# Kernel tuning notes

Hardware: AMD Instinct MI355X
Metric: run time of the kernel (lower is better)

Reference implementation:

```python
import jax, jax.numpy as jnp
import numpy as np

N = 100000        # nodes per batch
B = 1             # batch_size
E = 3200000       # edges
IN_F = 128        # in_features
ATT = 128         # attention_dim
HEADS = 8
DK = ATT // HEADS
SLOPE = 0.2       # leaky_relu_slope


def setup_inputs() -> dict:
    key = jax.random.key(0)
    k1, k2, k3, k4 = jax.random.split(key, 4)
    x = jax.random.normal(k1, (B * N, IN_F), dtype=jnp.float32)
    edge = jax.random.randint(k2, (B, 2, E), 0, N)
    # xavier_normal with gain=1.414 on W:[IN_F, ATT]
    W = jax.random.normal(k3, (IN_F, ATT), dtype=jnp.float32) * (1.414 * np.sqrt(2.0 / (IN_F + ATT)))
    # a originally [1, 2*d_k, 1, 1]; flattened to [2*d_k] (same math)
    a = jax.random.normal(k4, (2 * DK,), dtype=jnp.float32) * (1.414 * np.sqrt(2.0 / (2 * DK + 1)))
    return {"x": x, "edge": edge, "W": W, "a": a}


def _segment_softmax(scores, seg):
    # scores: [E, H], seg: [E] -> softmax within each segment (node id)
    smax = jax.ops.segment_max(scores, seg, num_segments=N)
    ex = jnp.exp(scores - smax[seg])
    denom = jax.ops.segment_sum(ex, seg, num_segments=N)
    return ex / denom[seg]


def reference(x, edge, W, a):
    wx = x @ W                                           # [B*N, ATT]
    h = wx.reshape(B, N, HEADS, DK).transpose(0, 1, 3, 2)  # [B, N, DK, H]
    a1, a2 = a[:DK], a[DK:]
    # sum(a * concat(h_src, h_dst)) = a1.h_src + a2.h_dst (linearity)
    s_src = jnp.einsum('bnkh,k->bnh', h, a1)             # [B, N, H]
    s_dst = jnp.einsum('bnkh,k->bnh', h, a2)             # [B, N, H]
    src = edge[:, 0, :]                                  # [B, E]
    dst = edge[:, 1, :]                                  # [B, E]
    gather = jax.vmap(lambda s, i: s[i])
    scores = gather(s_src, src) + gather(s_dst, dst)     # [B, E, H]
    edge_e = jnp.where(scores > 0, scores, SLOPE * scores)  # leaky relu
    # attention_norm_idx = 0 -> normalize over edges sharing a source node
    attention = jax.vmap(_segment_softmax)(edge_e, src)  # [B, E, H]
    return attention, wx
```

## Files before the change

### kernel.cpp

```cpp
#include <hip/hip_runtime.h>

#define N_NODES 100000
#define E_EDGES 3200000
#define IN_F 128
#define ATT 128
#define HEADS 8
#define DK 16
#define SLOPE 0.2f
#define NH (N_NODES * HEADS)

#define CHUNK 1792
#define NCHUNK 56
#define NSPLIT 9
#define QCAP 1016
#define SCAN_THREADS 512
#define ROUND_EDGES (SCAN_THREADS * 32)

__global__ __launch_bounds__(256) void gemm_s_kernel(
    const float* __restrict__ x, const float* __restrict__ W,
    const float* __restrict__ a, float* __restrict__ wx,
    float* __restrict__ s_src, float* __restrict__ s_dst)
{
    __shared__ float xs[8][128];
    __shared__ float Ws[8][128];

    const int tid = threadIdx.x;
    const int ty  = tid >> 4;
    const int tx  = tid & 15;
    const int row0 = blockIdx.x * 128;

    float acc[8][8];
#pragma unroll
    for (int i = 0; i < 8; i++)
#pragma unroll
        for (int j = 0; j < 8; j++) acc[i][j] = 0.f;

    const int lrow  = tid >> 1;
    const int khalf = (tid & 1) * 4;
    const int wkk   = tid >> 5;
    const int wc    = (tid & 31) * 4;

    for (int k0 = 0; k0 < IN_F; k0 += 8) {
        float4 xv = make_float4(0.f, 0.f, 0.f, 0.f);
        const int grow = row0 + lrow;
        if (grow < N_NODES)
            xv = *(const float4*)(x + (size_t)grow * IN_F + k0 + khalf);
        const float4 wv = *(const float4*)(W + (size_t)(k0 + wkk) * ATT + wc);

        __syncthreads();
        xs[khalf + 0][lrow] = xv.x;
        xs[khalf + 1][lrow] = xv.y;
        xs[khalf + 2][lrow] = xv.z;
        xs[khalf + 3][lrow] = xv.w;
        *(float4*)(&Ws[wkk][wc]) = wv;
        __syncthreads();

#pragma unroll
        for (int kk = 0; kk < 8; kk++) {
            float av[8], bv[8];
            *(float4*)(av)     = *(const float4*)(&xs[kk][ty * 8]);
            *(float4*)(av + 4) = *(const float4*)(&xs[kk][ty * 8 + 4]);
            *(float4*)(bv)     = *(const float4*)(&Ws[kk][tx * 8]);
            *(float4*)(bv + 4) = *(const float4*)(&Ws[kk][tx * 8 + 4]);
#pragma unroll
            for (int r = 0; r < 8; r++)
#pragma unroll
                for (int c = 0; c < 8; c++)
                    acc[r][c] = fmaf(av[r], bv[c], acc[r][c]);
        }
    }

    const int koff = (tx & 1) * 8;
    const int head = tx >> 1;
    float a1[8], a2[8];
#pragma unroll
    for (int c = 0; c < 8; c++) {
        a1[c] = a[koff + c];
        a2[c] = a[DK + koff + c];
    }

#pragma unroll
    for (int r = 0; r < 8; r++) {
        const int grow = row0 + ty * 8 + r;
        const bool ok = (grow < N_NODES);
        if (ok) {
            *(float4*)(wx + (size_t)grow * ATT + tx * 8) =
                make_float4(acc[r][0], acc[r][1], acc[r][2], acc[r][3]);
            *(float4*)(wx + (size_t)grow * ATT + tx * 8 + 4) =
                make_float4(acc[r][4], acc[r][5], acc[r][6], acc[r][7]);
        }
        float p1 = 0.f, p2 = 0.f;
#pragma unroll
        for (int c = 0; c < 8; c++) {
            p1 = fmaf(acc[r][c], a1[c], p1);
            p2 = fmaf(acc[r][c], a2[c], p2);
        }
        p1 += __shfl_xor(p1, 1);
        p2 += __shfl_xor(p2, 1);
        if (((tx & 1) == 0) && ok) {
            s_src[(size_t)grow * HEADS + head] = p1;
            s_dst[(size_t)grow * HEADS + head] = p2;
        }
    }
}

__global__ __launch_bounds__(SCAN_THREADS) void denom_scan_kernel(
    const int* __restrict__ src, const int* __restrict__ dst,
    const float* __restrict__ s_src, const float* __restrict__ s_dst,
    float* __restrict__ denoms)
{
    __shared__ float acc[HEADS][CHUNK + 1];
    __shared__ int qs[QCAP];
    __shared__ int qe[QCAP];
    __shared__ int qc;

    const int t    = threadIdx.x;
    const int lane = t & 63;
    const int lo   = blockIdx.x * CHUNK;
    const int hi   = min(lo + CHUNK, N_NODES);
    const int split = blockIdx.y;

    for (int i = t; i < HEADS * (CHUNK + 1); i += SCAN_THREADS)
        ((float*)acc)[i] = 0.f;
    if (t == 0) qc = 0;
    __syncthreads();

    const int per_split = (E_EDGES + NSPLIT - 1) / NSPLIT;
    const int e0 = split * per_split;
    const int e1 = min(e0 + per_split, E_EDGES);
    const int nrounds = (e1 - e0 + ROUND_EDGES - 1) / ROUND_EDGES;

    for (int r = 0; r < nrounds; r++) {
        const int rb = e0 + r * ROUND_EDGES;
#pragma unroll
        for (int u = 0; u < 8; u++) {
            const int e4 = rb + (u * SCAN_THREADS + t) * 4;
            int4 s4 = make_int4(-1, -1, -1, -1);
            if (e4 < e1) s4 = *(const int4*)(src + e4);
            const int ss[4] = {s4.x, s4.y, s4.z, s4.w};
#pragma unroll
            for (int j = 0; j < 4; j++) {
                const int s = ss[j];
                const bool hit = (s >= lo) && (s < hi);
                const unsigned long long m = __ballot(hit);
                if (m) {
                    const int leader = __ffsll((long long)m) - 1;
                    int wb = 0;
                    if (lane == leader) wb = atomicAdd(&qc, __popcll(m));
                    wb = __shfl(wb, leader);
                    if (hit) {
                        const int idx = wb + __popcll(m & ((1ull << lane) - 1ull));
                        if (idx < QCAP) { qs[idx] = s; qe[idx] = e4 + j; }
                        else {
                            const int d = dst[e4 + j];
                            const float4* ps = (const float4*)(s_src + (size_t)s * HEADS);
                            const float4* pd = (const float4*)(s_dst + (size_t)d * HEADS);
                            const float4 a0 = ps[0], a1 = ps[1], b0 = pd[0], b1 = pd[1];
                            const float sc[8] = {a0.x + b0.x, a0.y + b0.y, a0.z + b0.z, a0.w + b0.w,
                                                 a1.x + b1.x, a1.y + b1.y, a1.z + b1.z, a1.w + b1.w};
#pragma unroll
                            for (int h = 0; h < 8; h++) {
                                float v = sc[h];
                                v = v > 0.f ? v : SLOPE * v;
                                atomicAdd(&acc[h][s - lo], __expf(v));
                            }
                        }
                    }
                }
            }
        }
        __syncthreads();
        const int nq = min(qc, QCAP);
        for (int base = 0; base < nq; base += SCAN_THREADS) {
            const int i = base + t;
            if (i < nq) {
                const int s = qs[i];
                const int d = dst[qe[i]];
                const float4* ps = (const float4*)(s_src + (size_t)s * HEADS);
                const float4* pd = (const float4*)(s_dst + (size_t)d * HEADS);
                const float4 a0 = ps[0], a1 = ps[1], b0 = pd[0], b1 = pd[1];
                const float sc[8] = {a0.x + b0.x, a0.y + b0.y, a0.z + b0.z, a0.w + b0.w,
                                     a1.x + b1.x, a1.y + b1.y, a1.z + b1.z, a1.w + b1.w};
#pragma unroll
                for (int h = 0; h < 8; h++) {
                    float v = sc[h];
                    v = v > 0.f ? v : SLOPE * v;
                    atomicAdd(&acc[h][s - lo], __expf(v));
                }
            }
        }
        __syncthreads();
        if (t == 0) qc = 0;
        __syncthreads();
    }

    const int cnt = (hi - lo) * HEADS;
    float* outp = denoms + (size_t)split * NH + (size_t)lo * HEADS;
    for (int i = t; i < cnt; i += SCAN_THREADS)
        outp[i] = acc[i & 7][i >> 3];
}

__global__ __launch_bounds__(256) void reduce_recip_kernel(float* __restrict__ denoms)
{
    const int i = blockIdx.x * 256 + threadIdx.x;
    if (i >= NH) return;
    float s = 0.f;
#pragma unroll
    for (int c = 0; c < NSPLIT; c++) s += denoms[(size_t)c * NH + i];
    denoms[i] = __frcp_rn(s);
}

__global__ __launch_bounds__(256) void norm_kernel(
    const int* __restrict__ src, const int* __restrict__ dst,
    const float* __restrict__ s_src, const float* __restrict__ s_dst,
    const float* __restrict__ rdenom, float* __restrict__ att)
{
    const int e = blockIdx.x * 256 + threadIdx.x;
    if (e >= E_EDGES) return;
    const int s = src[e];
    const int d = dst[e];
    const float4* ps = (const float4*)(s_src + (size_t)s * HEADS);
    const float4* pd = (const float4*)(s_dst + (size_t)d * HEADS);
    const float4 s0 = ps[0], s1 = ps[1], d0 = pd[0], d1 = pd[1];
    const float4* pr = (const float4*)(rdenom + (size_t)s * HEADS);
    const float4 r0 = pr[0], r1 = pr[1];
    float sc[8] = {s0.x + d0.x, s0.y + d0.y, s0.z + d0.z, s0.w + d0.w,
                   s1.x + d1.x, s1.y + d1.y, s1.z + d1.z, s1.w + d1.w};
    float rd[8] = {r0.x, r0.y, r0.z, r0.w, r1.x, r1.y, r1.z, r1.w};
    float o[8];
#pragma unroll
    for (int h = 0; h < 8; h++) {
        float v = sc[h];
        v = v > 0.f ? v : SLOPE * v;
        o[h] = __expf(v) * rd[h];
    }
    float4* po = (float4*)(att + (size_t)e * HEADS);
    po[0] = make_float4(o[0], o[1], o[2], o[3]);
    po[1] = make_float4(o[4], o[5], o[6], o[7]);
}

extern "C" void kernel_launch(void* const* d_in, const int* in_sizes, int n_in,
                              void* d_out, int out_size, void* d_ws, size_t ws_size,
                              hipStream_t stream)
{
    const float* x    = (const float*)d_in[0];
    const int*   edge = (const int*)d_in[1];
    const float* W    = (const float*)d_in[2];
    const float* a    = (const float*)d_in[3];

    float* out = (float*)d_out;
    float* att = out;
    float* wx  = out + (size_t)E_EDGES * HEADS;

    float* ws     = (float*)d_ws;
    float* s_src  = ws;
    float* s_dst  = s_src + (size_t)NH;
    float* denoms = s_dst + (size_t)NH;

    const int* src = edge;
    const int* dst = edge + E_EDGES;

    const int gemm_blocks = (N_NODES + 127) / 128;
    gemm_s_kernel<<<gemm_blocks, 256, 0, stream>>>(x, W, a, wx, s_src, s_dst);

    dim3 sgrid(NCHUNK, NSPLIT);
    denom_scan_kernel<<<sgrid, SCAN_THREADS, 0, stream>>>(src, dst, s_src, s_dst, denoms);

    const int nblocks = (NH + 255) / 256;
    reduce_recip_kernel<<<nblocks, 256, 0, stream>>>(denoms);

    const int eblocks = (E_EDGES + 255) / 256;
    norm_kernel<<<eblocks, 256, 0, stream>>>(src, dst, s_src, s_dst, denoms, att);
}
```

Baseline: 654.4 us.

## Bin edges by source chunk with histogram/scan/scatter before denominator accumulation

Replaces the per-chunk full edge scan, where each of the 56x9 blocks rereads all source indices and filters by ballot, with a counting-sort style binning. A histogram, prefix scan and scatter write packed (local src, dst) words into the attention output buffer as scratch. The denominator kernel then reads only its own bin's edges and accumulates exp scores in shared memory. This removes the redundant rereads of the edge array but adds three extra launches, a single-block scan, and scattered global writes.

```diff
diff --git a/kernel.cpp b/kernel.cpp
--- a/kernel.cpp
+++ b/kernel.cpp
@@ -9,12 +9,11 @@
 #define SLOPE 0.2f
 #define NH (N_NODES * HEADS)
 
-#define CHUNK 1792
-#define NCHUNK 56
-#define NSPLIT 9
-#define QCAP 1016
-#define SCAN_THREADS 512
-#define ROUND_EDGES (SCAN_THREADS * 32)
+#define CHUNK 896
+#define NBINS 112
+#define NS 8
+#define HB 512
+#define EPB 6272
 
 __global__ __launch_bounds__(256) void gemm_s_kernel(
     const float* __restrict__ x, const float* __restrict__ W,
@@ -104,100 +103,150 @@
     }
 }
 
-__global__ __launch_bounds__(SCAN_THREADS) void denom_scan_kernel(
+__global__ __launch_bounds__(256) void hist_kernel(
+    const int* __restrict__ src, int* __restrict__ counts)
+{
+    __shared__ int h[NBINS];
+    const int t = threadIdx.x;
+    const int b = blockIdx.x;
+    for (int i = t; i < NBINS; i += 256) h[i] = 0;
+    __syncthreads();
+
+    const int rb = b * EPB;
+    const int re = min(rb + EPB, E_EDGES);
+    for (int i = rb + t * 4; i < re; i += 256 * 4) {
+        const int4 s4 = *(const int4*)(src + i);
+        atomicAdd(&h[s4.x / CHUNK], 1);
+        atomicAdd(&h[s4.y / CHUNK], 1);
+        atomicAdd(&h[s4.z / CHUNK], 1);
+        atomicAdd(&h[s4.w / CHUNK], 1);
+    }
+    __syncthreads();
+    for (int i = t; i < NBINS; i += 256) counts[i * HB + b] = h[i];
+}
+
+__global__ __launch_bounds__(1024) void scan_kernel(
+    const int* __restrict__ counts, int* __restrict__ offs)
+{
+    __shared__ int part[1024];
+    const int t = threadIdx.x;
+    const int per = (NBINS * HB) / 1024;
+    const int base = t * per;
+
+    int sum = 0;
+    for (int i = 0; i < per; i++) sum += counts[base + i];
+    part[t] = sum;
+    __syncthreads();
+
+    for (int off = 1; off < 1024; off <<= 1) {
+        int v = 0;
+        if (t >= off) v = part[t - off];
+        __syncthreads();
+        if (t >= off) part[t] += v;
+        __syncthreads();
+    }
+
+    int run = (t == 0) ? 0 : part[t - 1];
+    for (int i = 0; i < per; i++) {
+        offs[base + i] = run;
+        run += counts[base + i];
+    }
+}
+
+__global__ __launch_bounds__(256) void scatter_kernel(
     const int* __restrict__ src, const int* __restrict__ dst,
+    const int* __restrict__ offs, unsigned int* __restrict__ binned)
+{
+    __shared__ int cur[NBINS];
+    const int t = threadIdx.x;
+    const int b = blockIdx.x;
+    for (int i = t; i < NBINS; i += 256) cur[i] = offs[i * HB + b];
+    __syncthreads();
+
+    const int rb = b * EPB;
+    const int re = min(rb + EPB, E_EDGES);
+    for (int i = rb + t * 4; i < re; i += 256 * 4) {
+        const int4 s4 = *(const int4*)(src + i);
+        const int4 d4 = *(const int4*)(dst + i);
+        const int ss[4] = {s4.x, s4.y, s4.z, s4.w};
+        const int dd[4] = {d4.x, d4.y, d4.z, d4.w};
+#pragma unroll
+        for (int j = 0; j < 4; j++) {
+            const int c = ss[j] / CHUNK;
+            const int pos = atomicAdd(&cur[c], 1);
+            binned[pos] = ((unsigned int)(ss[j] - c * CHUNK) << 17) |
+                          (unsigned int)dd[j];
+        }
+    }
+}
+
+__global__ __launch_bounds__(256, 4) void denom_binned_kernel(
+    const unsigned int* __restrict__ binned, const int* __restrict__ offs,
     const float* __restrict__ s_src, const float* __restrict__ s_dst,
     float* __restrict__ denoms)
 {
     __shared__ float acc[HEADS][CHUNK + 1];
-    __shared__ int qs[QCAP];
-    __shared__ int qe[QCAP];
-    __shared__ int qc;
-
-    const int t    = threadIdx.x;
-    const int lane = t & 63;
-    const int lo   = blockIdx.x * CHUNK;
-    const int hi   = min(lo + CHUNK, N_NODES);
-    const int split = blockIdx.y;
-
-    for (int i = t; i < HEADS * (CHUNK + 1); i += SCAN_THREADS)
+
+    const int t  = threadIdx.x;
+    const int c  = blockIdx.x;
+    const int j  = blockIdx.y;
+    const int lo = c * CHUNK;
+    const int hi = min(lo + CHUNK, N_NODES);
+
+    for (int i = t; i < HEADS * (CHUNK + 1); i += 256)
         ((float*)acc)[i] = 0.f;
-    if (t == 0) qc = 0;
-    __syncthreads();
-
-    const int per_split = (E_EDGES + NSPLIT - 1) / NSPLIT;
-    const int e0 = split * per_split;
-    const int e1 = min(e0 + per_split, E_EDGES);
-    const int nrounds = (e1 - e0 + ROUND_EDGES - 1) / ROUND_EDGES;
-
-    for (int r = 0; r < nrounds; r++) {
-        const int rb = e0 + r * ROUND_EDGES;
-#pragma unroll
-        for (int u = 0; u < 8; u++) {
-            const int e4 = rb + (u * SCAN_THREADS + t) * 4;
-            int4 s4 = make_int4(-1, -1, -1, -1);
-            if (e4 < e1) s4 = *(const int4*)(src + e4);
-            const int ss[4] = {s4.x, s4.y, s4.z, s4.w};
-#pragma unroll
-            for (int j = 0; j < 4; j++) {
-                const int s = ss[j];
-                const bool hit = (s >= lo) && (s < hi);
-                const unsigned long long m = __ballot(hit);
-                if (m) {
-                    const int leader = __ffsll((long long)m) - 1;
-                    int wb = 0;
-                    if (lane == leader) wb = atomicAdd(&qc, __popcll(m));
-                    wb = __shfl(wb, leader);
-                    if (hit) {
-                        const int idx = wb + __popcll(m & ((1ull << lane) - 1ull));
-                        if (idx < QCAP) { qs[idx] = s; qe[idx] = e4 + j; }
-                        else {
-                            const int d = dst[e4 + j];
-                            const float4* ps = (const float4*)(s_src + (size_t)s * HEADS);
-                            const float4* pd = (const float4*)(s_dst + (size_t)d * HEADS);
-                            const float4 a0 = ps[0], a1 = ps[1], b0 = pd[0], b1 = pd[1];
-                            const float sc[8] = {a0.x + b0.x, a0.y + b0.y, a0.z + b0.z, a0.w + b0.w,
-                                                 a1.x + b1.x, a1.y + b1.y, a1.z + b1.z, a1.w + b1.w};
-#pragma unroll
-                            for (int h = 0; h < 8; h++) {
-                                float v = sc[h];
-                                v = v > 0.f ? v : SLOPE * v;
-                                atomicAdd(&acc[h][s - lo], __expf(v));
-                            }
-                        }
-                    }
-                }
-            }
-        }
-        __syncthreads();
-        const int nq = min(qc, QCAP);
-        for (int base = 0; base < nq; base += SCAN_THREADS) {
-            const int i = base + t;
-            if (i < nq) {
-                const int s = qs[i];
-                const int d = dst[qe[i]];
-                const float4* ps = (const float4*)(s_src + (size_t)s * HEADS);
-                const float4* pd = (const float4*)(s_dst + (size_t)d * HEADS);
-                const float4 a0 = ps[0], a1 = ps[1], b0 = pd[0], b1 = pd[1];
-                const float sc[8] = {a0.x + b0.x, a0.y + b0.y, a0.z + b0.z, a0.w + b0.w,
-                                     a1.x + b1.x, a1.y + b1.y, a1.z + b1.z, a1.w + b1.w};
-#pragma unroll
-                for (int h = 0; h < 8; h++) {
-                    float v = sc[h];
-                    v = v > 0.f ? v : SLOPE * v;
-                    atomicAdd(&acc[h][s - lo], __expf(v));
-                }
-            }
-        }
-        __syncthreads();
-        if (t == 0) qc = 0;
-        __syncthreads();
-    }
+    __syncthreads();
+
+    const int start = offs[c * HB];
+    const int end   = (c + 1 < NBINS) ? offs[(c + 1) * HB] : E_EDGES;
+    const int len   = end - start;
+    const int e0 = start + (int)((long long)len * j / NS);
+    const int e1 = start + (int)((long long)len * (j + 1) / NS);
+
+    int i = e0 + t;
+    for (; i + 256 < e1; i += 512) {
+        const unsigned int w0 = binned[i];
+        const unsigned int w1 = binned[i + 256];
+        const int di0 = w0 & 0x1FFFF, sl0 = w0 >> 17;
+        const int di1 = w1 & 0x1FFFF, sl1 = w1 >> 17;
+        const float4* ps0 = (const float4*)(s_src + (size_t)(lo + sl0) * HEADS);
+        const float4* pd0 = (const float4*)(s_dst + (size_t)di0 * HEADS);
+        const float4* ps1 = (const float4*)(s_src + (size_t)(lo + sl1) * HEADS);
+        const float4* pd1 = (const float4*)(s_dst + (size_t)di1 * HEADS);
+        const float4 xa0 = ps0[0], xa1 = ps0[1], xb0 = pd0[0], xb1 = pd0[1];
+        const float4 ya0 = ps1[0], ya1 = ps1[1], yb0 = pd1[0], yb1 = pd1[1];
+        const float s0[8] = {xa0.x + xb0.x, xa0.y + xb0.y, xa0.z + xb0.z, xa0.w + xb0.w,
+                             xa1.x + xb1.x, xa1.y + xb1.y, xa1.z + xb1.z, xa1.w + xb1.w};
+        const float s1[8] = {ya0.x + yb0.x, ya0.y + yb0.y, ya0.z + yb0.z, ya0.w + yb0.w,
+                             ya1.x + yb1.x, ya1.y + yb1.y, ya1.z + yb1.z, ya1.w + yb1.w};
+#pragma unroll
+        for (int h = 0; h < 8; h++) {
+            float v0 = s0[h]; v0 = v0 > 0.f ? v0 : SLOPE * v0;
+            float v1 = s1[h]; v1 = v1 > 0.f ? v1 : SLOPE * v1;
+            atomicAdd(&acc[h][sl0], __expf(v0));
+            atomicAdd(&acc[h][sl1], __expf(v1));
+        }
+    }
+    if (i < e1) {
+        const unsigned int w0 = binned[i];
+        const int di0 = w0 & 0x1FFFF, sl0 = w0 >> 17;
+        const float4* ps0 = (const float4*)(s_src + (size_t)(lo + sl0) * HEADS);
+        const float4* pd0 = (const float4*)(s_dst + (size_t)di0 * HEADS);
+        const float4 xa0 = ps0[0], xa1 = ps0[1], xb0 = pd0[0], xb1 = pd0[1];
+        const float s0[8] = {xa0.x + xb0.x, xa0.y + xb0.y, xa0.z + xb0.z, xa0.w + xb0.w,
+                             xa1.x + xb1.x, xa1.y + xb1.y, xa1.z + xb1.z, xa1.w + xb1.w};
+#pragma unroll
+        for (int h = 0; h < 8; h++) {
+            float v0 = s0[h]; v0 = v0 > 0.f ? v0 : SLOPE * v0;
+            atomicAdd(&acc[h][sl0], __expf(v0));
+        }
+    }
+    __syncthreads();
 
     const int cnt = (hi - lo) * HEADS;
-    float* outp = denoms + (size_t)split * NH + (size_t)lo * HEADS;
-    for (int i = t; i < cnt; i += SCAN_THREADS)
-        outp[i] = acc[i & 7][i >> 3];
+    float* outp = denoms + (size_t)j * NH + (size_t)lo * HEADS;
+    for (int i2 = t; i2 < cnt; i2 += 256)
+        outp[i2] = acc[i2 & 7][i2 >> 3];
 }
 
 __global__ __launch_bounds__(256) void reduce_recip_kernel(float* __restrict__ denoms)
@@ -206,7 +255,7 @@
     if (i >= NH) return;
     float s = 0.f;
 #pragma unroll
-    for (int c = 0; c < NSPLIT; c++) s += denoms[(size_t)c * NH + i];
+    for (int c = 0; c < NS; c++) s += denoms[(size_t)c * NH + i];
     denoms[i] = __frcp_rn(s);
 }
 
@@ -256,6 +305,10 @@
     float* s_src  = ws;
     float* s_dst  = s_src + (size_t)NH;
     float* denoms = s_dst + (size_t)NH;
+    int*   counts = (int*)(denoms + (size_t)NS * NH);
+    int*   offs   = counts + (size_t)NBINS * HB;
+
+    unsigned int* binned = (unsigned int*)att;
 
     const int* src = edge;
     const int* dst = edge + E_EDGES;
@@ -263,8 +316,12 @@
     const int gemm_blocks = (N_NODES + 127) / 128;
     gemm_s_kernel<<<gemm_blocks, 256, 0, stream>>>(x, W, a, wx, s_src, s_dst);
 
-    dim3 sgrid(NCHUNK, NSPLIT);
-    denom_scan_kernel<<<sgrid, SCAN_THREADS, 0, stream>>>(src, dst, s_src, s_dst, denoms);
+    hist_kernel<<<HB, 256, 0, stream>>>(src, counts);
+    scan_kernel<<<1, 1024, 0, stream>>>(counts, offs);
+    scatter_kernel<<<HB, 256, 0, stream>>>(src, dst, offs, binned);
+
+    dim3 bgrid(NBINS, NS);
+    denom_binned_kernel<<<bgrid, 256, 0, stream>>>(binned, offs, s_src, s_dst, denoms);
 
     const int nblocks = (NH + 255) / 256;
     reduce_recip_kernel<<<nblocks, 256, 0, stream>>>(denoms);
```

Result: faster. 551.0 us (-15.8%).

## Replace chunked scan with fused exp-store and global atomic denominators

Applied to the files above, without the earlier changes.

Replaces the per-chunk edge scan (which rereads the source array once per node chunk) with a single pass per edge. That pass computes exp scores, stores them to the output, and accumulates softmax denominators via global float atomics. A later pass multiplies the stored values by reciprocal denominators. This removes repeated edge scanning and the split reduction, at the cost of an extra read/write of the attention output and heavy contended global atomics.

```diff
diff --git a/kernel.cpp b/kernel.cpp
--- a/kernel.cpp
+++ b/kernel.cpp
@@ -9,13 +9,6 @@
 #define SLOPE 0.2f
 #define NH (N_NODES * HEADS)
 
-#define CHUNK 1792
-#define NCHUNK 56
-#define NSPLIT 9
-#define QCAP 1016
-#define SCAN_THREADS 512
-#define ROUND_EDGES (SCAN_THREADS * 32)
-
 __global__ __launch_bounds__(256) void gemm_s_kernel(
     const float* __restrict__ x, const float* __restrict__ W,
     const float* __restrict__ a, float* __restrict__ wx,
@@ -104,139 +97,89 @@
     }
 }
 
-__global__ __launch_bounds__(SCAN_THREADS) void denom_scan_kernel(
+__global__ __launch_bounds__(256) void zero_kernel(float4* __restrict__ p)
+{
+    const int i = blockIdx.x * 256 + threadIdx.x;
+    if (i < NH / 4) p[i] = make_float4(0.f, 0.f, 0.f, 0.f);
+}
+
+__global__ __launch_bounds__(256) void edge_fused_kernel(
     const int* __restrict__ src, const int* __restrict__ dst,
     const float* __restrict__ s_src, const float* __restrict__ s_dst,
-    float* __restrict__ denoms)
-{
-    __shared__ float acc[HEADS][CHUNK + 1];
-    __shared__ int qs[QCAP];
-    __shared__ int qe[QCAP];
-    __shared__ int qc;
-
-    const int t    = threadIdx.x;
-    const int lane = t & 63;
-    const int lo   = blockIdx.x * CHUNK;
-    const int hi   = min(lo + CHUNK, N_NODES);
-    const int split = blockIdx.y;
-
-    for (int i = t; i < HEADS * (CHUNK + 1); i += SCAN_THREADS)
-        ((float*)acc)[i] = 0.f;
-    if (t == 0) qc = 0;
-    __syncthreads();
-
-    const int per_split = (E_EDGES + NSPLIT - 1) / NSPLIT;
-    const int e0 = split * per_split;
-    const int e1 = min(e0 + per_split, E_EDGES);
-    const int nrounds = (e1 - e0 + ROUND_EDGES - 1) / ROUND_EDGES;
-
-    for (int r = 0; r < nrounds; r++) {
-        const int rb = e0 + r * ROUND_EDGES;
-#pragma unroll
-        for (int u = 0; u < 8; u++) {
-            const int e4 = rb + (u * SCAN_THREADS + t) * 4;
-            int4 s4 = make_int4(-1, -1, -1, -1);
-            if (e4 < e1) s4 = *(const int4*)(src + e4);
-            const int ss[4] = {s4.x, s4.y, s4.z, s4.w};
-#pragma unroll
-            for (int j = 0; j < 4; j++) {
-                const int s = ss[j];
-                const bool hit = (s >= lo) && (s < hi);
-                const unsigned long long m = __ballot(hit);
-                if (m) {
-                    const int leader = __ffsll((long long)m) - 1;
-                    int wb = 0;
-                    if (lane == leader) wb = atomicAdd(&qc, __popcll(m));
-                    wb = __shfl(wb, leader);
-                    if (hit) {
-                        const int idx = wb + __popcll(m & ((1ull << lane) - 1ull));
-                        if (idx < QCAP) { qs[idx] = s; qe[idx] = e4 + j; }
-                        else {
-                            const int d = dst[e4 + j];
-                            const float4* ps = (const float4*)(s_src + (size_t)s * HEADS);
-                            const float4* pd = (const float4*)(s_dst + (size_t)d * HEADS);
-                            const float4 a0 = ps[0], a1 = ps[1], b0 = pd[0], b1 = pd[1];
-                            const float sc[8] = {a0.x + b0.x, a0.y + b0.y, a0.z + b0.z, a0.w + b0.w,
-                                                 a1.x + b1.x, a1.y + b1.y, a1.z + b1.z, a1.w + b1.w};
-#pragma unroll
-                            for (int h = 0; h < 8; h++) {
-                                float v = sc[h];
-                                v = v > 0.f ? v : SLOPE * v;
-                                atomicAdd(&acc[h][s - lo], __expf(v));
-                            }
-                        }
-                    }
-                }
-            }
-        }
-        __syncthreads();
-        const int nq = min(qc, QCAP);
-        for (int base = 0; base < nq; base += SCAN_THREADS) {
-            const int i = base + t;
-            if (i < nq) {
-                const int s = qs[i];
-                const int d = dst[qe[i]];
-                const float4* ps = (const float4*)(s_src + (size_t)s * HEADS);
-                const float4* pd = (const float4*)(s_dst + (size_t)d * HEADS);
-                const float4 a0 = ps[0], a1 = ps[1], b0 = pd[0], b1 = pd[1];
-                const float sc[8] = {a0.x + b0.x, a0.y + b0.y, a0.z + b0.z, a0.w + b0.w,
-                                     a1.x + b1.x, a1.y + b1.y, a1.z + b1.z, a1.w + b1.w};
-#pragma unroll
-                for (int h = 0; h < 8; h++) {
-                    float v = sc[h];
-                    v = v > 0.f ? v : SLOPE * v;
-                    atomicAdd(&acc[h][s - lo], __expf(v));
-                }
-            }
-        }
-        __syncthreads();
-        if (t == 0) qc = 0;
-        __syncthreads();
-    }
-
-    const int cnt = (hi - lo) * HEADS;
-    float* outp = denoms + (size_t)split * NH + (size_t)lo * HEADS;
-    for (int i = t; i < cnt; i += SCAN_THREADS)
-        outp[i] = acc[i & 7][i >> 3];
-}
-
-__global__ __launch_bounds__(256) void reduce_recip_kernel(float* __restrict__ denoms)
+    float* __restrict__ denoms, float* __restrict__ att)
+{
+    const int e0 = (blockIdx.x * 256 + threadIdx.x) * 2;
+    if (e0 >= E_EDGES) return;
+    const int2 sp = *(const int2*)(src + e0);
+    const int2 dp = *(const int2*)(dst + e0);
+
+    const float4* ps0 = (const float4*)(s_src + (size_t)sp.x * HEADS);
+    const float4* ps1 = (const float4*)(s_src + (size_t)sp.y * HEADS);
+    const float4* pd0 = (const float4*)(s_dst + (size_t)dp.x * HEADS);
+    const float4* pd1 = (const float4*)(s_dst + (size_t)dp.y * HEADS);
+    const float4 xa0 = ps0[0], xa1 = ps0[1];
+    const float4 ya0 = ps1[0], ya1 = ps1[1];
+    const float4 xb0 = pd0[0], xb1 = pd0[1];
+    const float4 yb0 = pd1[0], yb1 = pd1[1];
+
+    const float s0[8] = {xa0.x + xb0.x, xa0.y + xb0.y, xa0.z + xb0.z, xa0.w + xb0.w,
+                         xa1.x + xb1.x, xa1.y + xb1.y, xa1.z + xb1.z, xa1.w + xb1.w};
+    const float s1[8] = {ya0.x + yb0.x, ya0.y + yb0.y, ya0.z + yb0.z, ya0.w + yb0.w,
+                         ya1.x + yb1.x, ya1.y + yb1.y, ya1.z + yb1.z, ya1.w + yb1.w};
+    float ex0[8], ex1[8];
+#pragma unroll
+    for (int h = 0; h < 8; h++) {
+        float v = s0[h]; v = v > 0.f ? v : SLOPE * v;
+        ex0[h] = __expf(v);
+        float u = s1[h]; u = u > 0.f ? u : SLOPE * u;
+        ex1[h] = __expf(u);
+    }
+
+    float4* pa = (float4*)(att + (size_t)e0 * HEADS);
+    pa[0] = make_float4(ex0[0], ex0[1], ex0[2], ex0[3]);
+    pa[1] = make_float4(ex0[4], ex0[5], ex0[6], ex0[7]);
+    pa[2] = make_float4(ex1[0], ex1[1], ex1[2], ex1[3]);
+    pa[3] = make_float4(ex1[4], ex1[5], ex1[6], ex1[7]);
+
+    float* q0 = denoms + (size_t)sp.x * HEADS;
+    float* q1 = denoms + (size_t)sp.y * HEADS;
+#pragma unroll
+    for (int h = 0; h < 8; h++) {
+        unsafeAtomicAdd(q0 + h, ex0[h]);
+        unsafeAtomicAdd(q1 + h, ex1[h]);
+    }
+}
+
+__global__ __launch_bounds__(256) void reduce_recip_kernel(
+    const float* __restrict__ denoms, float* __restrict__ rdenom)
 {
     const int i = blockIdx.x * 256 + threadIdx.x;
     if (i >= NH) return;
-    float s = 0.f;
-#pragma unroll
-    for (int c = 0; c < NSPLIT; c++) s += denoms[(size_t)c * NH + i];
-    denoms[i] = __frcp_rn(s);
-}
-
-__global__ __launch_bounds__(256) void norm_kernel(
-    const int* __restrict__ src, const int* __restrict__ dst,
-    const float* __restrict__ s_src, const float* __restrict__ s_dst,
-    const float* __restrict__ rdenom, float* __restrict__ att)
-{
-    const int e = blockIdx.x * 256 + threadIdx.x;
-    if (e >= E_EDGES) return;
-    const int s = src[e];
-    const int d = dst[e];
-    const float4* ps = (const float4*)(s_src + (size_t)s * HEADS);
-    const float4* pd = (const float4*)(s_dst + (size_t)d * HEADS);
-    const float4 s0 = ps[0], s1 = ps[1], d0 = pd[0], d1 = pd[1];
-    const float4* pr = (const float4*)(rdenom + (size_t)s * HEADS);
-    const float4 r0 = pr[0], r1 = pr[1];
-    float sc[8] = {s0.x + d0.x, s0.y + d0.y, s0.z + d0.z, s0.w + d0.w,
-                   s1.x + d1.x, s1.y + d1.y, s1.z + d1.z, s1.w + d1.w};
-    float rd[8] = {r0.x, r0.y, r0.z, r0.w, r1.x, r1.y, r1.z, r1.w};
-    float o[8];
-#pragma unroll
-    for (int h = 0; h < 8; h++) {
-        float v = sc[h];
-        v = v > 0.f ? v : SLOPE * v;
-        o[h] = __expf(v) * rd[h];
-    }
-    float4* po = (float4*)(att + (size_t)e * HEADS);
-    po[0] = make_float4(o[0], o[1], o[2], o[3]);
-    po[1] = make_float4(o[4], o[5], o[6], o[7]);
+    rdenom[i] = __frcp_rn(denoms[i]);
+}
+
+__global__ __launch_bounds__(256) void norm_mul_kernel(
+    const int* __restrict__ src, const float* __restrict__ rdenom,
+    float* __restrict__ att)
+{
+    const int e0 = (blockIdx.x * 256 + threadIdx.x) * 2;
+    if (e0 >= E_EDGES) return;
+    const int2 sp = *(const int2*)(src + e0);
+
+    const float4* r0 = (const float4*)(rdenom + (size_t)sp.x * HEADS);
+    const float4* r1 = (const float4*)(rdenom + (size_t)sp.y * HEADS);
+    const float4 ra0 = r0[0], ra1 = r0[1];
+    const float4 rb0 = r1[0], rb1 = r1[1];
+
+    float4* pa = (float4*)(att + (size_t)e0 * HEADS);
+    float4 x0 = pa[0], x1 = pa[1], x2 = pa[2], x3 = pa[3];
+
+    x0.x *= ra0.x; x0.y *= ra0.y; x0.z *= ra0.z; x0.w *= ra0.w;
+    x1.x *= ra1.x; x1.y *= ra1.y; x1.z *= ra1.z; x1.w *= ra1.w;
+    x2.x *= rb0.x; x2.y *= rb0.y; x2.z *= rb0.z; x2.w *= rb0.w;
+    x3.x *= rb1.x; x3.y *= rb1.y; x3.z *= rb1.z; x3.w *= rb1.w;
+
+    pa[0] = x0; pa[1] = x1; pa[2] = x2; pa[3] = x3;
 }
 
 extern "C" void kernel_launch(void* const* d_in, const int* in_sizes, int n_in,
@@ -256,19 +199,22 @@
     float* s_src  = ws;
     float* s_dst  = s_src + (size_t)NH;
     float* denoms = s_dst + (size_t)NH;
+    float* rdenom = denoms + (size_t)NH;
 
     const int* src = edge;
     const int* dst = edge + E_EDGES;
 
+    zero_kernel<<<(NH / 4 + 255) / 256, 256, 0, stream>>>((float4*)denoms);
+
     const int gemm_blocks = (N_NODES + 127) / 128;
     gemm_s_kernel<<<gemm_blocks, 256, 0, stream>>>(x, W, a, wx, s_src, s_dst);
 
-    dim3 sgrid(NCHUNK, NSPLIT);
-    denom_scan_kernel<<<sgrid, SCAN_THREADS, 0, stream>>>(src, dst, s_src, s_dst, denoms);
+    const int eblocks = (E_EDGES / 2 + 255) / 256;
+    edge_fused_kernel<<<eblocks, 256, 0, stream>>>(src, dst, s_src, s_dst,
+                                                   denoms, att);
 
     const int nblocks = (NH + 255) / 256;
-    reduce_recip_kernel<<<nblocks, 256, 0, stream>>>(denoms);
-
-    const int eblocks = (E_EDGES + 255) / 256;
-    norm_kernel<<<eblocks, 256, 0, stream>>>(src, dst, s_src, s_dst, denoms, att);
-}
+    reduce_recip_kernel<<<nblocks, 256, 0, stream>>>(denoms, rdenom);
+
+    norm_mul_kernel<<<eblocks, 256, 0, stream>>>(src, rdenom, att);
+}
```

Result: slower. 1.571 ms (+140.1%).
